# Optimization experiments

Hardware: AMD Instinct MI355X
Metric: run time of the kernel (lower is better)

Reference implementation:

```python
import jax, jax.numpy as jnp
import numpy as np

BSZ, SEQ, DIM, NH = 2, 2048, 2048, 16
HD = DIM // NH  # 128


def setup_inputs() -> dict:
    key = jax.random.key(0)
    ks = jax.random.split(key, 6)
    x = jax.random.normal(ks[0], (BSZ, SEQ, DIM), dtype=jnp.float32)
    # torch Linear weights: [out_features, in_features]
    scale = 1.0 / np.sqrt(DIM)
    wq = jax.random.normal(ks[1], (DIM, DIM), dtype=jnp.float32) * scale
    wk = jax.random.normal(ks[2], (DIM, DIM), dtype=jnp.float32) * scale
    wv = jax.random.normal(ks[3], (DIM, DIM), dtype=jnp.float32) * scale
    wo = jax.random.normal(ks[4], (DIM, DIM), dtype=jnp.float32) * scale
    # RoPE freqs (llama style): theta=10000
    inv_freq = 1.0 / (10000.0 ** (jnp.arange(0, HD, 2, dtype=jnp.float32) / HD))  # [HD//2]
    t = jnp.arange(SEQ, dtype=jnp.float32)
    angles = jnp.outer(t, inv_freq)  # [SEQ, HD//2]
    freqs_cos = jnp.cos(angles)
    freqs_sin = jnp.sin(angles)
    # causal additive mask [SEQ, SEQ]
    mask = jnp.where(jnp.tril(jnp.ones((SEQ, SEQ), dtype=bool)), 0.0, -jnp.inf).astype(jnp.float32)
    return {"x": x, "wq": wq, "wk": wk, "wv": wv, "wo": wo,
            "freqs_cos": freqs_cos, "freqs_sin": freqs_sin, "mask": mask}


def _apply_rope(v, cos, sin):
    # v: [b, s, h, hd]; complex pairs are interleaved (even=real, odd=imag)
    b, s, h, hd = v.shape
    vr = v.reshape(b, s, h, hd // 2, 2)
    v0, v1 = vr[..., 0], vr[..., 1]
    c = cos[None, :, None, :]  # [1, s, 1, hd//2]
    sn = sin[None, :, None, :]
    out = jnp.stack([v0 * c - v1 * sn, v0 * sn + v1 * c], axis=-1)
    return out.reshape(b, s, h, hd)


def reference(x, wq, wk, wv, wo, freqs_cos, freqs_sin, mask):
    b, s, _ = x.shape
    xq = (x @ wq.T).reshape(b, s, NH, HD)
    xk = (x @ wk.T).reshape(b, s, NH, HD)
    xv = (x @ wv.T).reshape(b, s, NH, HD)
    xq = _apply_rope(xq, freqs_cos, freqs_sin)
    xk = _apply_rope(xk, freqs_cos, freqs_sin)
    # [b, h, s, s]
    scores = jnp.einsum('bqhd,bkhd->bhqk', xq, xk) / jnp.sqrt(jnp.float32(HD))
    scores = scores + mask[None, None, :, :]
    probs = jax.nn.softmax(scores.astype(jnp.float32), axis=-1).astype(scores.dtype)
    out = jnp.einsum('bhqk,bkhd->bqhd', probs, xv).reshape(b, s, NH * HD)
    return out @ wo.T
```

## Files before the change

### kernel.cpp

```cpp
#include <hip/hip_runtime.h>
#include <hip/hip_bf16.h>
#include <stdint.h>

typedef __bf16 bf16x8 __attribute__((ext_vector_type(8)));
typedef float f32x4 __attribute__((ext_vector_type(4)));
typedef unsigned short u16;
typedef unsigned int u32;

#define DEVI __device__ __forceinline__

DEVI u16 f2b(float f){ __bf16 h = (__bf16)f; return __builtin_bit_cast(u16, h); }
DEVI float b2f(u16 u){ return (float)__builtin_bit_cast(__bf16, u); }

constexpr int BSZ = 2, SEQ = 2048, DIM = 2048, NH = 16, HD = 128;

#if defined(__has_builtin)
#if __has_builtin(__builtin_amdgcn_global_load_lds)
#define HAVE_ASYNC_LDS 1
#endif
#endif

DEVI void cp16(void* lds, const void* g){
#ifdef HAVE_ASYNC_LDS
  auto gp = (const __attribute__((address_space(1))) u32*)(uintptr_t)g;
  auto lp = (__attribute__((address_space(3))) u32*)(uintptr_t)lds;
  __builtin_amdgcn_global_load_lds(gp, lp, 16, 0, 0);
#else
  *(uint4*)lds = *(const uint4*)g;
#endif
}

__global__ __launch_bounds__(256) void k_convert(
    const float* __restrict__ x, const float* __restrict__ wq,
    const float* __restrict__ wk, const float* __restrict__ wv,
    const float* __restrict__ wo,
    u16* __restrict__ xb, u16* __restrict__ wqkv, u16* __restrict__ wob)
{
  int e = (blockIdx.x * 256 + threadIdx.x) * 4;
  float4 v; u16* dp;
  if (e < 8388608){
    v = *(const float4*)&x[e]; dp = &xb[e];
  } else if (e < 20971520){
    int o = e - 8388608; int sec = o >> 22; int oo = o & 4194303;
    const float* w = (sec == 0) ? wq : ((sec == 1) ? wk : wv);
    v = *(const float4*)&w[oo]; dp = &wqkv[o];
  } else {
    int o = e - 20971520;
    v = *(const float4*)&wo[o]; dp = &wob[o];
  }
  ushort4 r; r.x = f2b(v.x); r.y = f2b(v.y); r.z = f2b(v.z); r.w = f2b(v.w);
  *(ushort4*)dp = r;
}

DEVI void gemm_core_256x128(u16* smem, const u16* __restrict__ A, const u16* __restrict__ B,
                            int tm, int tn, int t, f32x4 (&acc)[4][4])
{
  const int lane = t & 63, l15 = lane & 15, quad = lane >> 4;
  const int wave = t >> 6, wm = wave >> 1, wn = wave & 1;
  const int swr = (l15 & 7) << 3;
  const int rb = t >> 3;
  const int csw = ((t & 7) ^ (rb & 7)) << 3;
  const u16* As0 = A + (size_t)(tm + rb) * DIM + csw;
  const u16* Bs0 = B + (size_t)(tn + rb) * DIM + csw;

  auto STAGE = [&](int kt){
    const int buf = kt & 1;
    const int kb = kt * 64;
    u16* d = &smem[buf * 24576 + t * 8];
    #pragma unroll
    for (int p = 0; p < 4; ++p)
      cp16(d + p * 4096, As0 + (size_t)p * (64 * DIM) + kb);
    #pragma unroll
    for (int p = 0; p < 2; ++p)
      cp16(d + 16384 + p * 4096, Bs0 + (size_t)p * (64 * DIM) + kb);
  };

  STAGE(0);
  #pragma unroll 2
  for (int kt = 0; kt < DIM / 64; ++kt){
    __syncthreads();
    if (kt < DIM / 64 - 1) STAGE(kt + 1);
    const u16* Ab = &smem[(kt & 1) * 24576];
    const u16* Bb = Ab + 16384;
    bf16x8 Af[4][2], Bf[4][2];
    #pragma unroll
    for (int mt = 0; mt < 4; ++mt)
      #pragma unroll
      for (int ks = 0; ks < 2; ++ks)
        Af[mt][ks] = *(const bf16x8*)&Ab[(wm * 64 + mt * 16 + l15) * 64 + ((ks * 32 + quad * 8) ^ swr)];
    #pragma unroll
    for (int nt = 0; nt < 4; ++nt)
      #pragma unroll
      for (int ks = 0; ks < 2; ++ks)
        Bf[nt][ks] = *(const bf16x8*)&Bb[(wn * 64 + nt * 16 + l15) * 64 + ((ks * 32 + quad * 8) ^ swr)];
    #pragma unroll
    for (int c = 0; c < 4; ++c){
      const int mb = (c >> 1) * 2, nb = (c & 1) * 2;
      __builtin_amdgcn_s_setprio(1);
      #pragma unroll
      for (int mi = 0; mi < 2; ++mi)
        #pragma unroll
        for (int ni = 0; ni < 2; ++ni)
          #pragma unroll
          for (int ks = 0; ks < 2; ++ks)
            acc[mb + mi][nb + ni] = __builtin_amdgcn_mfma_f32_16x16x32_bf16(
                Af[mb + mi][ks], Bf[nb + ni][ks], acc[mb + mi][nb + ni], 0, 0, 0);
      __builtin_amdgcn_s_setprio(0);
    }
  }
  __syncthreads();
}

__global__ __launch_bounds__(512, 2) void k_gemm_qkv(
    const u16* __restrict__ A, const u16* __restrict__ W,
    const float* __restrict__ fc, const float* __restrict__ fs,
    u16* __restrict__ Qd, u16* __restrict__ Kd, u16* __restrict__ Vt)
{
  __shared__ __align__(16) u16 smem[49152];
  const int t = threadIdx.x;
  const int wg = blockIdx.x;
  const int id = (wg & 7) * 96 + (wg >> 3);
  const int tm = (id & 15) << 8;
  const int tn = (id >> 4) << 7;
  f32x4 acc[4][4] = {};
  gemm_core_256x128(smem, A, W, tm, tn, t, acc);

  const int lane = t & 63, l15 = lane & 15, quad = lane >> 4;
  const int wave = t >> 6, wm = wave >> 1, wn = wave & 1;
  u16* Cs = smem;
  #pragma unroll
  for (int mt = 0; mt < 4; ++mt)
    #pragma unroll
    for (int nt = 0; nt < 4; ++nt)
      #pragma unroll
      for (int r = 0; r < 4; ++r){
        int rin = wm * 64 + mt * 16 + quad * 4 + r;
        int col = wn * 64 + nt * 16 + l15;
        Cs[rin * 128 + ((col + rin * 8) & 127)] = f2b(acc[mt][nt][r]);
      }
  __syncthreads();

  const int sec = tn >> 11;
  const int hh = (tn & 2047) >> 7;
  if (sec < 2){
    u16* dst = (sec == 0) ? Qd : Kd;
    const float qs = (sec == 0) ? (0.08838834764831845f * 1.4426950408889634f) : 1.0f;
    const int col0 = (t & 15) * 8;
    #pragma unroll
    for (int jj = 0; jj < 8; ++jj){
      int row = (t >> 4) + jj * 32;
      int m = tm + row;
      int b = m >> 11, s = m & 2047;
      uint4 cv = *(const uint4*)&Cs[row * 128 + ((col0 + row * 8) & 127)];
      const u16* cp = (const u16*)&cv;
      u16 op[8];
      float4 c4 = *(const float4*)&fc[(size_t)s * 64 + (col0 >> 1)];
      float4 s4 = *(const float4*)&fs[(size_t)s * 64 + (col0 >> 1)];
      float cc[4] = {c4.x*qs, c4.y*qs, c4.z*qs, c4.w*qs};
      float ss[4] = {s4.x*qs, s4.y*qs, s4.z*qs, s4.w*qs};
      #pragma unroll
      for (int p = 0; p < 4; ++p){
        float a = b2f(cp[2*p]), bb = b2f(cp[2*p+1]);
        op[2*p]   = f2b(a*cc[p] - bb*ss[p]);
        op[2*p+1] = f2b(a*ss[p] + bb*cc[p]);
      }
      *(uint4*)&dst[((size_t)(b*NH + hh)*SEQ + s)*HD + col0] = *(const uint4*)op;
    }
  } else {
    const int bb = tm >> 11;
    const int sbase = tm & 2047;
    const size_t baseT = ((size_t)(bb*NH + hh)) * HD * SEQ;
    const int d0 = (t & 15) * 8;
    const int s0g = (t >> 4) * 8;
    u16 tr[8][8];
    #pragma unroll
    for (int jr = 0; jr < 8; ++jr){
      int row = s0g + jr;
      *(uint4*)&tr[jr][0] = *(const uint4*)&Cs[row * 128 + ((d0 + row * 8) & 127)];
    }
    #pragma unroll
    for (int jd = 0; jd < 8; ++jd){
      u16 o[8];
      #pragma unroll
      for (int jr = 0; jr < 8; ++jr) o[jr] = tr[jr][jd];
      *(uint4*)&Vt[baseT + (size_t)(d0 + jd)*SEQ + sbase + s0g] = *(const uint4*)o;
    }
  }
}

__global__ __launch_bounds__(512) void k_flash(
    const u16* __restrict__ Qd, const u16* __restrict__ Kd,
    const u16* __restrict__ Vt, u16* __restrict__ OP0, u16* __restrict__ OP1,
    float* __restrict__ Mp, float* __restrict__ Lp)
{
  __shared__ __align__(16) u16 lds[40960];
  const int t = threadIdx.x, lane = t & 63, wave = t >> 6;
  const int l15 = lane & 15, quad = lane >> 4;
  const int swz = (l15 & 7) << 3;

  const int flat = blockIdx.x;
  const int xcd = flat & 7, idx = flat >> 3;
  const int bh = xcd * 4 + (idx >> 4);
  const int x = idx & 15;
  const int b = bh >> 4, h = bh & 15;
  const int j = x >> 1, split = x & 1;

  const size_t base  = (size_t)bh * SEQ * HD;
  const size_t baseT = (size_t)bh * HD * SEQ;
  u16* Psw = lds + 32768 + wave * 1024;
  u16* OPs = split ? OP1 : OP0;
  const int lo = 17*split, hi = lo + 17;
  const int qt0 = j, qt1 = 15 - j;
  const int len0 = 2*qt0 + 2;

  const int krow = t >> 4, kslot = t & 15;
  const int vrow = t >> 3, vslot = t & 7;

  for (int pass = 0; pass < 2; ++pass){
    const int qt = pass ? qt1 : qt0;
    const int len = 2*qt + 2;
    int kt0 = pass ? (lo - len0) : lo; if (kt0 < 0) kt0 = 0;
    int kt1 = pass ? (hi - len0) : hi; if (kt1 > len) kt1 = len;
    const int qb = qt*128 + wave*16;

    bf16x8 qf[4];
    #pragma unroll
    for (int ks = 0; ks < 4; ++ks)
      qf[ks] = *(const bf16x8*)&Qd[base + (size_t)(qb + l15)*HD + ks*32 + quad*8];

    f32x4 oacc[8] = {};
    float m_s = -1e30f, l_s = 0.f;

    if (kt0 < kt1){
      uint4 kreg[2], vreg[2];
      auto LOADT = [&](int kt){
        #pragma unroll
        for (int i = 0; i < 2; ++i){
          kreg[i] = *(const uint4*)&Kd[base + (size_t)(kt*64 + i*32 + krow)*HD + kslot*8];
          vreg[i] = *(const uint4*)&Vt[baseT + (size_t)(i*64 + vrow)*SEQ + kt*64 + vslot*8];
        }
      };
      auto WRITET = [&](int bu){
        u16* Kb = lds + bu*8192;
        u16* Vb = lds + 16384 + bu*8192;
        #pragma unroll
        for (int i = 0; i < 2; ++i){
          int kr = i*32 + krow;
          *(uint4*)&Kb[kr*128 + ((kslot*8) ^ ((kr & 7) << 3))] = kreg[i];
          int vr = i*64 + vrow;
          *(uint4*)&Vb[vr*64 + ((vslot*8) ^ ((vr & 7) << 3))] = vreg[i];
        }
      };
      LOADT(kt0);
      WRITET(0);
      if (kt0 + 1 < kt1) LOADT(kt0 + 1);
      __syncthreads();
      int buf = 0;
      for (int kt = kt0; kt < kt1; ++kt){
        if (kt*64 <= qb + 15){
          const u16* Kb = lds + buf*8192;
          const u16* Vb = lds + 16384 + buf*8192;
          f32x4 sacc[4] = {};
          #pragma unroll
          for (int ks = 0; ks < 4; ++ks){
            bf16x8 kf[4];
            #pragma unroll
            for (int nk = 0; nk < 4; ++nk)
              kf[nk] = *(const bf16x8*)&Kb[(nk*16 + l15)*128 + ((ks*32 + quad*8) ^ swz)];
            __builtin_amdgcn_s_setprio(1);
            #pragma unroll
            for (int nk = 0; nk < 4; ++nk)
              sacc[nk] = __builtin_amdgcn_mfma_f32_16x16x32_bf16(kf[nk], qf[ks], sacc[nk], 0, 0, 0);
            __builtin_amdgcn_s_setprio(0);
          }
          if (kt*64 + 63 > qb){
            int q = qb + l15;
            #pragma unroll
            for (int nk = 0; nk < 4; ++nk)
              #pragma unroll
              for (int r = 0; r < 4; ++r){
                int key = kt*64 + nk*16 + quad*4 + r;
                if (key > q) sacc[nk][r] = -1e30f;
              }
          }
          float m4[4];
          #pragma unroll
          for (int nk = 0; nk < 4; ++nk)
            m4[nk] = fmaxf(fmaxf(sacc[nk][0], sacc[nk][1]), fmaxf(sacc[nk][2], sacc[nk][3]));
          float rm = fmaxf(fmaxf(m4[0], m4[1]), fmaxf(m4[2], m4[3]));
          rm = fmaxf(rm, __shfl_xor(rm, 16));
          rm = fmaxf(rm, __shfl_xor(rm, 32));
          if (__ballot(rm > m_s) != 0){
            float mnew = fmaxf(m_s, rm);
            float alpha = exp2f(m_s - mnew);
            m_s = mnew;
            l_s *= alpha;
            #pragma unroll
            for (int db = 0; db < 8; ++db)
              #pragma unroll
              for (int r = 0; r < 4; ++r) oacc[db][r] *= alpha;
          }
          float s4[4];
          #pragma unroll
          for (int nk = 0; nk < 4; ++nk){
            u16 pk[4];
            float p0 = exp2f(sacc[nk][0] - m_s);
            float p1 = exp2f(sacc[nk][1] - m_s);
            float p2 = exp2f(sacc[nk][2] - m_s);
            float p3 = exp2f(sacc[nk][3] - m_s);
            pk[0] = f2b(p0); pk[1] = f2b(p1); pk[2] = f2b(p2); pk[3] = f2b(p3);
            s4[nk] = (p0 + p1) + (p2 + p3);
            *(uint2*)&Psw[l15*64 + ((nk*16 + quad*4) ^ swz)] = *(const uint2*)pk;
          }
          float rs = (s4[0] + s4[1]) + (s4[2] + s4[3]);
          rs += __shfl_xor(rs, 16);
          rs += __shfl_xor(rs, 32);
          l_s += rs;
          #pragma unroll
          for (int k2 = 0; k2 < 2; ++k2){
            bf16x8 pf = *(const bf16x8*)&Psw[l15*64 + ((k2*32 + quad*8) ^ swz)];
            __builtin_amdgcn_s_setprio(1);
            #pragma unroll
            for (int db = 0; db < 8; ++db){
              bf16x8 vf = *(const bf16x8*)&Vb[(db*16 + l15)*64 + ((k2*32 + quad*8) ^ swz)];
              oacc[db] = __builtin_amdgcn_mfma_f32_16x16x32_bf16(vf, pf, oacc[db], 0, 0, 0);
            }
            __builtin_amdgcn_s_setprio(0);
          }
        }
        if (kt + 1 < kt1){
          WRITET(buf ^ 1);
          if (kt + 2 < kt1) LOADT(kt + 2);
          __syncthreads();
        }
        buf ^= 1;
      }
    }
    {
      u16* Ow = Psw;
      const int qrow = lane >> 2;
      #pragma unroll
      for (int ch = 0; ch < 2; ++ch){
        #pragma unroll
        for (int db2 = 0; db2 < 4; ++db2){
          int db = ch*4 + db2;
          u16 ok[4];
          #pragma unroll
          for (int r = 0; r < 4; ++r) ok[r] = f2b(oacc[db][r]);
          *(uint2*)&Ow[l15*64 + ((db2*16 + quad*4) ^ swz)] = *(const uint2*)ok;
        }
        #pragma unroll
        for (int i = 0; i < 2; ++i){
          int c8 = (lane & 3) + i*4;
          uint4 v = *(const uint4*)&Ow[qrow*64 + ((c8*8) ^ ((qrow & 7) << 3))];
          *(uint4*)&OPs[(((size_t)(b*SEQ + qb + qrow))*NH + h)*HD + ch*64 + c8*8] = v;
        }
      }
      if (quad == 0){
        size_t mi = ((size_t)split*BSZ*NH + bh)*SEQ + (qb + l15);
        Mp[mi] = m_s;
        Lp[mi] = l_s;
      }
    }
    __syncthreads();
  }
}

__global__ __launch_bounds__(256) void k_combine(
    u16* __restrict__ OP0, const u16* __restrict__ OP1,
    const float* __restrict__ Mp, const float* __restrict__ Lp)
{
  size_t flat = ((size_t)blockIdx.x*256 + threadIdx.x)*8;
  int h = (int)((flat >> 7) & 15);
  int s = (int)((flat >> 11) & 2047);
  int b = (int)(flat >> 22);
  size_t row = ((size_t)(b*NH + h))*SEQ + s;
  const size_t off1 = (size_t)BSZ*NH*SEQ;
  float m0 = Mp[row], l0 = Lp[row];
  float m1 = Mp[row + off1], l1 = Lp[row + off1];
  float m = fmaxf(m0, m1);
  float w0 = exp2f(m0 - m), w1 = exp2f(m1 - m);
  float inv = 1.0f / (w0*l0 + w1*l1);
  uint4 a = *(const uint4*)&OP0[flat];
  uint4 c = *(const uint4*)&OP1[flat];
  const u16* pa = (const u16*)&a;
  const u16* pc = (const u16*)&c;
  u16 o[8];
  #pragma unroll
  for (int i = 0; i < 8; ++i)
    o[i] = f2b((b2f(pa[i])*w0 + b2f(pc[i])*w1) * inv);
  *(uint4*)&OP0[flat] = *(const uint4*)o;
}

__global__ __launch_bounds__(512, 2) void k_gemm_out(
    const u16* __restrict__ A, const u16* __restrict__ W, float* __restrict__ out)
{
  __shared__ __align__(16) u16 smem[49152];
  const int t = threadIdx.x;
  const int wg = blockIdx.x;
  const int id = (wg & 7) * 32 + (wg >> 3);
  const int tm = (id & 15) << 8;
  const int tn = (id >> 4) << 7;
  f32x4 acc[4][4] = {};
  gemm_core_256x128(smem, A, W, tm, tn, t, acc);
  const int lane = t & 63, l15 = lane & 15, quad = lane >> 4;
  const int wave = t >> 6, wm = wave >> 1, wn = wave & 1;
  #pragma unroll
  for (int mt = 0; mt < 4; ++mt)
    #pragma unroll
    for (int nt = 0; nt < 4; ++nt)
      #pragma unroll
      for (int r = 0; r < 4; ++r){
        int row = tm + wm*64 + mt*16 + quad*4 + r;
        int col = tn + wn*64 + nt*16 + l15;
        out[(size_t)row*DIM + col] = acc[mt][nt][r];
      }
}

extern "C" void kernel_launch(void* const* d_in, const int* in_sizes, int n_in,
                              void* d_out, int out_size, void* d_ws, size_t ws_size,
                              hipStream_t stream)
{
  const float* x  = (const float*)d_in[0];
  const float* wq = (const float*)d_in[1];
  const float* wk = (const float*)d_in[2];
  const float* wv = (const float*)d_in[3];
  const float* wo = (const float*)d_in[4];
  const float* fc = (const float*)d_in[5];
  const float* fs = (const float*)d_in[6];
  float* out = (float*)d_out;

  char* ws = (char*)d_ws;
  u16* xb   = (u16*)(ws);
  u16* wqkv = (u16*)(ws + 16777216);
  u16* wob  = (u16*)(ws + 41943040);
  u16* Qr   = (u16*)(ws + 50331648);
  u16* Kr   = (u16*)(ws + 67108864);
  u16* VtT  = (u16*)(ws + 83886080);
  u16* Ob   = (u16*)(ws + 100663296);
  u16* OP1  = wqkv;
  float* Mp = (float*)(ws + 33554432);
  float* Lp = (float*)(ws + 34078720);

  k_convert <<<24576, 256, 0, stream>>>(x, wq, wk, wv, wo, xb, wqkv, wob);
  k_gemm_qkv<<<768, 512, 0, stream>>>(xb, wqkv, fc, fs, Qr, Kr, VtT);
  k_flash   <<<512, 512, 0, stream>>>(Qr, Kr, VtT, Ob, OP1, Mp, Lp);
  k_combine <<<4096, 256, 0, stream>>>(Ob, OP1, Mp, Lp);
  k_gemm_out<<<256, 512, 0, stream>>>(Ob, wob, out);
}
```

Measured before the change: 429.8 us.

## Switch flash attention to 32x32x16 MFMA with in-register P via permlane swap

Rewrites the flash kernel around 32x32x16 bf16 MFMAs, with each of 4 waves owning 32 query rows instead of 8 waves owning 16. The softmax probabilities are packed to bf16 and moved into the B-operand layout with v_permlane32_swap instead of a round trip through LDS. The block shrinks to 256 threads and the per-wave P scratch in LDS is removed. The aim is fewer LDS accesses and fewer MFMA issues per tile, at the cost of more registers per wave and fewer waves per block.

```diff
diff --git a/kernel.cpp b/kernel.cpp
--- a/kernel.cpp
+++ b/kernel.cpp
@@ -4,6 +4,7 @@
 
 typedef __bf16 bf16x8 __attribute__((ext_vector_type(8)));
 typedef float f32x4 __attribute__((ext_vector_type(4)));
+typedef float f32x16 __attribute__((ext_vector_type(16)));
 typedef unsigned short u16;
 typedef unsigned int u32;
 
@@ -188,15 +189,15 @@
   }
 }
 
-__global__ __launch_bounds__(512) void k_flash(
+__global__ __launch_bounds__(256) void k_flash(
     const u16* __restrict__ Qd, const u16* __restrict__ Kd,
     const u16* __restrict__ Vt, u16* __restrict__ OP0, u16* __restrict__ OP1,
     float* __restrict__ Mp, float* __restrict__ Lp)
 {
-  __shared__ __align__(16) u16 lds[40960];
+  __shared__ __align__(16) u16 lds[32768];
   const int t = threadIdx.x, lane = t & 63, wave = t >> 6;
-  const int l15 = lane & 15, quad = lane >> 4;
-  const int swz = (l15 & 7) << 3;
+  const int l31 = lane & 31, hi = lane >> 5;
+  const int swz = (lane & 7) << 3;
 
   const int flat = blockIdx.x;
   const int xcd = flat & 7, idx = flat >> 3;
@@ -207,9 +208,8 @@
 
   const size_t base  = (size_t)bh * SEQ * HD;
   const size_t baseT = (size_t)bh * HD * SEQ;
-  u16* Psw = lds + 32768 + wave * 1024;
   u16* OPs = split ? OP1 : OP0;
-  const int lo = 17*split, hi = lo + 17;
+  const int lo = 17*split, hi_t = lo + 17;
   const int qt0 = j, qt1 = 15 - j;
   const int len0 = 2*qt0 + 2;
 
@@ -220,35 +220,34 @@
     const int qt = pass ? qt1 : qt0;
     const int len = 2*qt + 2;
     int kt0 = pass ? (lo - len0) : lo; if (kt0 < 0) kt0 = 0;
-    int kt1 = pass ? (hi - len0) : hi; if (kt1 > len) kt1 = len;
-    const int qb = qt*128 + wave*16;
-
-    bf16x8 qf[4];
-    #pragma unroll
-    for (int ks = 0; ks < 4; ++ks)
-      qf[ks] = *(const bf16x8*)&Qd[base + (size_t)(qb + l15)*HD + ks*32 + quad*8];
-
-    f32x4 oacc[8] = {};
+    int kt1 = pass ? (hi_t - len0) : hi_t; if (kt1 > len) kt1 = len;
+    const int qb = qt*128 + wave*32;
+    const int q = qb + l31;
+
+    bf16x8 qf[8];
+    #pragma unroll
+    for (int ks = 0; ks < 8; ++ks)
+      qf[ks] = *(const bf16x8*)&Qd[base + (size_t)q*HD + ks*16 + hi*8];
+
+    f32x16 oacc[4] = {};
     float m_s = -1e30f, l_s = 0.f;
 
     if (kt0 < kt1){
-      uint4 kreg[2], vreg[2];
+      uint4 kreg[4], vreg[4];
       auto LOADT = [&](int kt){
         #pragma unroll
-        for (int i = 0; i < 2; ++i){
-          kreg[i] = *(const uint4*)&Kd[base + (size_t)(kt*64 + i*32 + krow)*HD + kslot*8];
-          vreg[i] = *(const uint4*)&Vt[baseT + (size_t)(i*64 + vrow)*SEQ + kt*64 + vslot*8];
+        for (int i = 0; i < 4; ++i){
+          kreg[i] = *(const uint4*)&Kd[base + (size_t)(kt*64 + i*16 + krow)*HD + kslot*8];
+          vreg[i] = *(const uint4*)&Vt[baseT + (size_t)(i*32 + vrow)*SEQ + kt*64 + vslot*8];
         }
       };
       auto WRITET = [&](int bu){
         u16* Kb = lds + bu*8192;
         u16* Vb = lds + 16384 + bu*8192;
         #pragma unroll
-        for (int i = 0; i < 2; ++i){
-          int kr = i*32 + krow;
-          *(uint4*)&Kb[kr*128 + ((kslot*8) ^ ((kr & 7) << 3))] = kreg[i];
-          int vr = i*64 + vrow;
-          *(uint4*)&Vb[vr*64 + ((vslot*8) ^ ((vr & 7) << 3))] = vreg[i];
+        for (int i = 0; i < 4; ++i){
+          *(uint4*)&Kb[(i*16 + krow)*128 + ((kslot*8) ^ ((krow & 7) << 3))] = kreg[i];
+          *(uint4*)&Vb[(i*32 + vrow)*64 + ((vslot*8) ^ ((vrow & 7) << 3))] = vreg[i];
         }
       };
       LOADT(kt0);
@@ -257,38 +256,32 @@
       __syncthreads();
       int buf = 0;
       for (int kt = kt0; kt < kt1; ++kt){
-        if (kt*64 <= qb + 15){
+        if (kt*64 <= qb + 31){
           const u16* Kb = lds + buf*8192;
           const u16* Vb = lds + 16384 + buf*8192;
-          f32x4 sacc[4] = {};
-          #pragma unroll
-          for (int ks = 0; ks < 4; ++ks){
-            bf16x8 kf[4];
+          f32x16 sacc0 = {}, sacc1 = {};
+          #pragma unroll
+          for (int ks = 0; ks < 8; ++ks){
+            bf16x8 kf0 = *(const bf16x8*)&Kb[l31*128 + ((ks*16 + hi*8) ^ swz)];
+            bf16x8 kf1 = *(const bf16x8*)&Kb[(32 + l31)*128 + ((ks*16 + hi*8) ^ swz)];
+            __builtin_amdgcn_s_setprio(1);
+            sacc0 = __builtin_amdgcn_mfma_f32_32x32x16_bf16(kf0, qf[ks], sacc0, 0, 0, 0);
+            sacc1 = __builtin_amdgcn_mfma_f32_32x32x16_bf16(kf1, qf[ks], sacc1, 0, 0, 0);
+            __builtin_amdgcn_s_setprio(0);
+          }
+          if (kt*64 + 63 > qb){
             #pragma unroll
-            for (int nk = 0; nk < 4; ++nk)
-              kf[nk] = *(const bf16x8*)&Kb[(nk*16 + l15)*128 + ((ks*32 + quad*8) ^ swz)];
-            __builtin_amdgcn_s_setprio(1);
-            #pragma unroll
-            for (int nk = 0; nk < 4; ++nk)
-              sacc[nk] = __builtin_amdgcn_mfma_f32_16x16x32_bf16(kf[nk], qf[ks], sacc[nk], 0, 0, 0);
-            __builtin_amdgcn_s_setprio(0);
-          }
-          if (kt*64 + 63 > qb){
-            int q = qb + l15;
-            #pragma unroll
-            for (int nk = 0; nk < 4; ++nk)
-              #pragma unroll
-              for (int r = 0; r < 4; ++r){
-                int key = kt*64 + nk*16 + quad*4 + r;
-                if (key > q) sacc[nk][r] = -1e30f;
-              }
-          }
-          float m4[4];
-          #pragma unroll
-          for (int nk = 0; nk < 4; ++nk)
-            m4[nk] = fmaxf(fmaxf(sacc[nk][0], sacc[nk][1]), fmaxf(sacc[nk][2], sacc[nk][3]));
-          float rm = fmaxf(fmaxf(m4[0], m4[1]), fmaxf(m4[2], m4[3]));
-          rm = fmaxf(rm, __shfl_xor(rm, 16));
+            for (int r = 0; r < 16; ++r){
+              int key0 = kt*64 + (r & 3) + 8*(r >> 2) + 4*hi;
+              if (key0 > q)      sacc0[r] = -1e30f;
+              if (key0 + 32 > q) sacc1[r] = -1e30f;
+            }
+          }
+          float rm = sacc0[0];
+          #pragma unroll
+          for (int r = 1; r < 16; ++r) rm = fmaxf(rm, sacc0[r]);
+          #pragma unroll
+          for (int r = 0; r < 16; ++r) rm = fmaxf(rm, sacc1[r]);
           rm = fmaxf(rm, __shfl_xor(rm, 32));
           if (__ballot(rm > m_s) != 0){
             float mnew = fmaxf(m_s, rm);
@@ -296,35 +289,52 @@
             m_s = mnew;
             l_s *= alpha;
             #pragma unroll
-            for (int db = 0; db < 8; ++db)
+            for (int db = 0; db < 4; ++db)
               #pragma unroll
-              for (int r = 0; r < 4; ++r) oacc[db][r] *= alpha;
-          }
-          float s4[4];
-          #pragma unroll
-          for (int nk = 0; nk < 4; ++nk){
-            u16 pk[4];
-            float p0 = exp2f(sacc[nk][0] - m_s);
-            float p1 = exp2f(sacc[nk][1] - m_s);
-            float p2 = exp2f(sacc[nk][2] - m_s);
-            float p3 = exp2f(sacc[nk][3] - m_s);
-            pk[0] = f2b(p0); pk[1] = f2b(p1); pk[2] = f2b(p2); pk[3] = f2b(p3);
-            s4[nk] = (p0 + p1) + (p2 + p3);
-            *(uint2*)&Psw[l15*64 + ((nk*16 + quad*4) ^ swz)] = *(const uint2*)pk;
-          }
-          float rs = (s4[0] + s4[1]) + (s4[2] + s4[3]);
-          rs += __shfl_xor(rs, 16);
+              for (int r = 0; r < 16; ++r) oacc[db][r] *= alpha;
+          }
+          float rs = 0.f;
+          #pragma unroll
+          for (int r = 0; r < 16; ++r){
+            sacc0[r] = exp2f(sacc0[r] - m_s);
+            sacc1[r] = exp2f(sacc1[r] - m_s);
+            rs += sacc0[r] + sacc1[r];
+          }
           rs += __shfl_xor(rs, 32);
           l_s += rs;
-          #pragma unroll
-          for (int k2 = 0; k2 < 2; ++k2){
-            bf16x8 pf = *(const bf16x8*)&Psw[l15*64 + ((k2*32 + quad*8) ^ swz)];
+          bf16x8 pf[4];
+          #pragma unroll
+          for (int kslot2 = 0; kslot2 < 4; ++kslot2){
+            const int q0 = (kslot2 & 1) * 8;
+            u32 w0, w1, w2, w3;
+            float p0, p1, p2, p3, p4, p5, p6, p7;
+            if (kslot2 < 2){
+              p0=sacc0[q0+0]; p1=sacc0[q0+1]; p2=sacc0[q0+2]; p3=sacc0[q0+3];
+              p4=sacc0[q0+4]; p5=sacc0[q0+5]; p6=sacc0[q0+6]; p7=sacc0[q0+7];
+            } else {
+              p0=sacc1[q0+0]; p1=sacc1[q0+1]; p2=sacc1[q0+2]; p3=sacc1[q0+3];
+              p4=sacc1[q0+4]; p5=sacc1[q0+5]; p6=sacc1[q0+6]; p7=sacc1[q0+7];
+            }
+            asm("v_cvt_pk_bf16_f32 %0, %1, %2" : "=v"(w0) : "v"(p0), "v"(p1));
+            asm("v_cvt_pk_bf16_f32 %0, %1, %2" : "=v"(w1) : "v"(p2), "v"(p3));
+            asm("v_cvt_pk_bf16_f32 %0, %1, %2" : "=v"(w2) : "v"(p4), "v"(p5));
+            asm("v_cvt_pk_bf16_f32 %0, %1, %2" : "=v"(w3) : "v"(p6), "v"(p7));
+            asm("v_permlane32_swap_b32 %0, %1" : "+v"(w0), "+v"(w2));
+            asm("v_permlane32_swap_b32 %0, %1" : "+v"(w1), "+v"(w3));
+            union { u32 w[4]; bf16x8 v; } u;
+            u.w[0] = w0; u.w[1] = w1; u.w[2] = w2; u.w[3] = w3;
+            pf[kslot2] = u.v;
+          }
+          #pragma unroll
+          for (int kslot2 = 0; kslot2 < 4; ++kslot2){
+            bf16x8 vf[4];
+            #pragma unroll
+            for (int db = 0; db < 4; ++db)
+              vf[db] = *(const bf16x8*)&Vb[(db*32 + l31)*64 + ((kslot2*16 + hi*8) ^ swz)];
             __builtin_amdgcn_s_setprio(1);
             #pragma unroll
-            for (int db = 0; db < 8; ++db){
-              bf16x8 vf = *(const bf16x8*)&Vb[(db*16 + l15)*64 + ((k2*32 + quad*8) ^ swz)];
-              oacc[db] = __builtin_amdgcn_mfma_f32_16x16x32_bf16(vf, pf, oacc[db], 0, 0, 0);
-            }
+            for (int db = 0; db < 4; ++db)
+              oacc[db] = __builtin_amdgcn_mfma_f32_32x32x16_bf16(vf[db], pf[kslot2], oacc[db], 0, 0, 0);
             __builtin_amdgcn_s_setprio(0);
           }
         }
@@ -336,28 +346,28 @@
         buf ^= 1;
       }
     }
+    __syncthreads();
     {
-      u16* Ow = Psw;
-      const int qrow = lane >> 2;
-      #pragma unroll
-      for (int ch = 0; ch < 2; ++ch){
+      u16* Osw = lds + wave*4096;
+      #pragma unroll
+      for (int db = 0; db < 4; ++db)
         #pragma unroll
-        for (int db2 = 0; db2 < 4; ++db2){
-          int db = ch*4 + db2;
-          u16 ok[4];
-          #pragma unroll
-          for (int r = 0; r < 4; ++r) ok[r] = f2b(oacc[db][r]);
-          *(uint2*)&Ow[l15*64 + ((db2*16 + quad*4) ^ swz)] = *(const uint2*)ok;
+        for (int rp = 0; rp < 8; ++rp){
+          int r0 = rp*2;
+          int d0 = db*32 + (r0 & 3) + 8*(r0 >> 2) + 4*hi;
+          u32 w = (u32)f2b(oacc[db][r0]) | ((u32)f2b(oacc[db][r0+1]) << 16);
+          int phys = (d0 & 7) + ((d0 & ~7) ^ ((l31 & 7) << 3));
+          *(u32*)&Osw[l31*128 + phys] = w;
         }
-        #pragma unroll
-        for (int i = 0; i < 2; ++i){
-          int c8 = (lane & 3) + i*4;
-          uint4 v = *(const uint4*)&Ow[qrow*64 + ((c8*8) ^ ((qrow & 7) << 3))];
-          *(uint4*)&OPs[(((size_t)(b*SEQ + qb + qrow))*NH + h)*HD + ch*64 + c8*8] = v;
-        }
-      }
-      if (quad == 0){
-        size_t mi = ((size_t)split*BSZ*NH + bh)*SEQ + (qb + l15);
+      #pragma unroll
+      for (int i = 0; i < 8; ++i){
+        int qr = i*4 + (lane >> 4);
+        int c0 = (lane & 15) * 8;
+        uint4 v = *(const uint4*)&Osw[qr*128 + (c0 ^ ((qr & 7) << 3))];
+        *(uint4*)&OPs[(((size_t)(b*SEQ + qb + qr))*NH + h)*HD + c0] = v;
+      }
+      if (lane < 32){
+        size_t mi = ((size_t)split*BSZ*NH + bh)*SEQ + q;
         Mp[mi] = m_s;
         Lp[mi] = l_s;
       }
@@ -444,7 +454,7 @@
 
   k_convert <<<24576, 256, 0, stream>>>(x, wq, wk, wv, wo, xb, wqkv, wob);
   k_gemm_qkv<<<768, 512, 0, stream>>>(xb, wqkv, fc, fs, Qr, Kr, VtT);
-  k_flash   <<<512, 512, 0, stream>>>(Qr, Kr, VtT, Ob, OP1, Mp, Lp);
+  k_flash   <<<512, 256, 0, stream>>>(Qr, Kr, VtT, Ob, OP1, Mp, Lp);
   k_combine <<<4096, 256, 0, stream>>>(Ob, OP1, Mp, Lp);
   k_gemm_out<<<256, 512, 0, stream>>>(Ob, wob, out);
 }
```

Measured after the change: 446.2 us. 1.04x slower.

## Fuse split-KV combine into output projection GEMM A-tile loading

Applied to the files above, without the earlier changes.

Removes the separate combine kernel and instead merges the two flash-attention partial outputs (rescaled by their max/sum statistics) while loading A tiles inside the output GEMM. The GEMM main loop is rewritten with register-prefetched A data and async-staged B tiles, double buffered in shared memory. This saves one kernel launch and a full read-modify-write pass over the attention output. The cost is that each GEMM block re-reads both partials plus M/L stats for every column tile (8 N-tiles), so partial-output traffic is duplicated and extra register pressure is added.

```diff
diff --git a/kernel.cpp b/kernel.cpp
--- a/kernel.cpp
+++ b/kernel.cpp
@@ -366,34 +366,10 @@
   }
 }
 
-__global__ __launch_bounds__(256) void k_combine(
-    u16* __restrict__ OP0, const u16* __restrict__ OP1,
-    const float* __restrict__ Mp, const float* __restrict__ Lp)
-{
-  size_t flat = ((size_t)blockIdx.x*256 + threadIdx.x)*8;
-  int h = (int)((flat >> 7) & 15);
-  int s = (int)((flat >> 11) & 2047);
-  int b = (int)(flat >> 22);
-  size_t row = ((size_t)(b*NH + h))*SEQ + s;
-  const size_t off1 = (size_t)BSZ*NH*SEQ;
-  float m0 = Mp[row], l0 = Lp[row];
-  float m1 = Mp[row + off1], l1 = Lp[row + off1];
-  float m = fmaxf(m0, m1);
-  float w0 = exp2f(m0 - m), w1 = exp2f(m1 - m);
-  float inv = 1.0f / (w0*l0 + w1*l1);
-  uint4 a = *(const uint4*)&OP0[flat];
-  uint4 c = *(const uint4*)&OP1[flat];
-  const u16* pa = (const u16*)&a;
-  const u16* pc = (const u16*)&c;
-  u16 o[8];
-  #pragma unroll
-  for (int i = 0; i < 8; ++i)
-    o[i] = f2b((b2f(pa[i])*w0 + b2f(pc[i])*w1) * inv);
-  *(uint4*)&OP0[flat] = *(const uint4*)o;
-}
-
 __global__ __launch_bounds__(512, 2) void k_gemm_out(
-    const u16* __restrict__ A, const u16* __restrict__ W, float* __restrict__ out)
+    const u16* __restrict__ OP0, const u16* __restrict__ OP1,
+    const float* __restrict__ Mp, const float* __restrict__ Lp,
+    const u16* __restrict__ W, float* __restrict__ out)
 {
   __shared__ __align__(16) u16 smem[49152];
   const int t = threadIdx.x;
@@ -401,10 +377,96 @@
   const int id = (wg & 7) * 32 + (wg >> 3);
   const int tm = (id & 15) << 8;
   const int tn = (id >> 4) << 7;
-  f32x4 acc[4][4] = {};
-  gemm_core_256x128(smem, A, W, tm, tn, t, acc);
+
   const int lane = t & 63, l15 = lane & 15, quad = lane >> 4;
   const int wave = t >> 6, wm = wave >> 1, wn = wave & 1;
+  const int swr = (l15 & 7) << 3;
+  const int rb = t >> 3;
+  const int csw = ((t & 7) ^ (rb & 7)) << 3;
+  const u16* Bs0 = W + (size_t)(tn + rb) * DIM + csw;
+  const size_t off1 = (size_t)BSZ * NH * SEQ;
+
+  auto STAGE_B = [&](int kt){
+    u16* d = &smem[(kt & 1) * 24576 + 16384 + t * 8];
+    #pragma unroll
+    for (int p = 0; p < 2; ++p)
+      cp16(d + p * 4096, Bs0 + (size_t)p * (64 * DIM) + kt * 64);
+  };
+
+  uint4 a0[4], a1[4];
+  float sm0[4], sl0[4], sm1[4], sl1[4];
+  auto PRE_A = [&](int kt){
+    const int kb = kt * 64;
+    const int hh = kb >> 7;
+    #pragma unroll
+    for (int p = 0; p < 4; ++p){
+      int row = tm + rb + p * 64;
+      size_t src = (size_t)row * DIM + kb + csw;
+      a0[p] = *(const uint4*)&OP0[src];
+      a1[p] = *(const uint4*)&OP1[src];
+      int b = row >> 11, s = row & 2047;
+      size_t mrow = ((size_t)(b * NH + hh)) * SEQ + s;
+      sm0[p] = Mp[mrow];        sl0[p] = Lp[mrow];
+      sm1[p] = Mp[mrow + off1]; sl1[p] = Lp[mrow + off1];
+    }
+  };
+  auto WRITE_A = [&](int kt){
+    u16* d = &smem[(kt & 1) * 24576 + t * 8];
+    #pragma unroll
+    for (int p = 0; p < 4; ++p){
+      float m = fmaxf(sm0[p], sm1[p]);
+      float w0 = exp2f(sm0[p] - m), w1 = exp2f(sm1[p] - m);
+      float inv = 1.0f / (w0 * sl0[p] + w1 * sl1[p]);
+      const u16* pa = (const u16*)&a0[p];
+      const u16* pc = (const u16*)&a1[p];
+      u16 o[8];
+      #pragma unroll
+      for (int i = 0; i < 8; ++i)
+        o[i] = f2b((b2f(pa[i]) * w0 + b2f(pc[i]) * w1) * inv);
+      *(uint4*)(d + p * 4096) = *(const uint4*)o;
+    }
+  };
+
+  f32x4 acc[4][4] = {};
+  PRE_A(0);
+  STAGE_B(0);
+  WRITE_A(0);
+  PRE_A(1);
+  for (int kt = 0; kt < DIM / 64; ++kt){
+    __syncthreads();
+    if (kt + 1 < DIM / 64) STAGE_B(kt + 1);
+    const u16* Ab = &smem[(kt & 1) * 24576];
+    const u16* Bb = Ab + 16384;
+    bf16x8 Af[4][2], Bf[4][2];
+    #pragma unroll
+    for (int mt = 0; mt < 4; ++mt)
+      #pragma unroll
+      for (int ks = 0; ks < 2; ++ks)
+        Af[mt][ks] = *(const bf16x8*)&Ab[(wm * 64 + mt * 16 + l15) * 64 + ((ks * 32 + quad * 8) ^ swr)];
+    #pragma unroll
+    for (int nt = 0; nt < 4; ++nt)
+      #pragma unroll
+      for (int ks = 0; ks < 2; ++ks)
+        Bf[nt][ks] = *(const bf16x8*)&Bb[(wn * 64 + nt * 16 + l15) * 64 + ((ks * 32 + quad * 8) ^ swr)];
+    #pragma unroll
+    for (int c = 0; c < 4; ++c){
+      const int mb = (c >> 1) * 2, nb = (c & 1) * 2;
+      __builtin_amdgcn_s_setprio(1);
+      #pragma unroll
+      for (int mi = 0; mi < 2; ++mi)
+        #pragma unroll
+        for (int ni = 0; ni < 2; ++ni)
+          #pragma unroll
+          for (int ks = 0; ks < 2; ++ks)
+            acc[mb + mi][nb + ni] = __builtin_amdgcn_mfma_f32_16x16x32_bf16(
+                Af[mb + mi][ks], Bf[nb + ni][ks], acc[mb + mi][nb + ni], 0, 0, 0);
+      __builtin_amdgcn_s_setprio(0);
+    }
+    if (kt + 1 < DIM / 64){
+      WRITE_A(kt + 1);
+      if (kt + 2 < DIM / 64) PRE_A(kt + 2);
+    }
+  }
   #pragma unroll
   for (int mt = 0; mt < 4; ++mt)
     #pragma unroll
@@ -445,6 +507,5 @@
   k_convert <<<24576, 256, 0, stream>>>(x, wq, wk, wv, wo, xb, wqkv, wob);
   k_gemm_qkv<<<768, 512, 0, stream>>>(xb, wqkv, fc, fs, Qr, Kr, VtT);
   k_flash   <<<512, 512, 0, stream>>>(Qr, Kr, VtT, Ob, OP1, Mp, Lp);
-  k_combine <<<4096, 256, 0, stream>>>(Ob, OP1, Mp, Lp);
-  k_gemm_out<<<256, 512, 0, stream>>>(Ob, wob, out);
-}
+  k_gemm_out<<<256, 512, 0, stream>>>(Ob, OP1, Mp, Lp, wob, out);
+}
```

Result: slower. 445.4 us (+3.6%).
